# Optimization experiments

Measured on AMD Instinct MI355X. Metric: run time of the kernel, lower is better.

## Reference

```python
import jax, jax.numpy as jnp
import numpy as np
import math

D = 1024
B, S = 8, 2048


def setup_inputs() -> dict:
    key = jax.random.key(0)
    ks = jax.random.split(key, 8)
    q = jax.random.normal(ks[0], (B, S, D), dtype=jnp.float32)
    k = jax.random.normal(ks[1], (B, S, D), dtype=jnp.float32)
    v1 = jax.random.normal(ks[2], (B, S, D), dtype=jnp.float32)
    mask = jax.random.normal(ks[3], (1, S, S), dtype=jnp.float32)
    # Linear params: torch Linear stores W as [out, in]; init ~ U(-1/sqrt(in), 1/sqrt(in))
    lim = 1.0 / math.sqrt(D)
    W1 = jax.random.uniform(ks[4], (D, D), jnp.float32, -lim, lim)
    b1 = jax.random.uniform(ks[5], (D,), jnp.float32, -lim, lim)
    W2 = jax.random.uniform(ks[6], (D, D), jnp.float32, -lim, lim)
    b2 = jax.random.uniform(ks[7], (D,), jnp.float32, -lim, lim)
    return {"q": q, "k": k, "v1": v1, "mask": mask,
            "W1": W1, "b1": b1, "W2": W2, "b2": b2}


def _proj(x, W1, b1, W2, b2):
    # linear2(linear1(x)); torch Linear: x @ W.T + b
    h = jnp.einsum('bsd,od->bso', x, W1) + b1
    return jnp.einsum('bsd,od->bso', h, W2) + b2


def reference(q, k, v1, mask, W1, b1, W2, b2):
    qp = _proj(q, W1, b1, W2, b2)          # [B,S,D]
    kp = _proj(k, W1, b1, W2, b2)          # [B,S,D]
    scale = 1.0 / math.sqrt(qp.shape[-1])
    qk = jnp.einsum('bqd,bkd->bqk', qp, kp) * scale  # [B,S,S]
    qk = qk + mask                          # broadcast [1,S,S]
    attn = jax.nn.softmax(qk, axis=-1)
    return jnp.einsum('bqk,bkd->bqd', attn, v1)  # [B,S,D]
```

## Files before the change

kernel.cpp:

```cpp
#include <hip/hip_runtime.h>
#include <hip/hip_bf16.h>

typedef __hip_bfloat16 bf16;
typedef __bf16 bf16x8 __attribute__((ext_vector_type(8)));
typedef float f32x4 __attribute__((ext_vector_type(4)));

constexpr int Bn = 8, Sn = 2048, Dn = 1024;
constexpr int BM = 256, BN = 256, BK = 64;

__global__ void cast_f32_bf16_k(const float* __restrict__ x, bf16* __restrict__ y, int n) {
  int i = (blockIdx.x * blockDim.x + threadIdx.x) * 4;
  if (i >= n) return;
  float4 f = *reinterpret_cast<const float4*>(x + i);
  bf16 tmp[4] = {__float2bfloat16(f.x), __float2bfloat16(f.y),
                 __float2bfloat16(f.z), __float2bfloat16(f.w)};
  *reinterpret_cast<short4*>(y + i) = *reinterpret_cast<const short4*>(tmp);
}

__global__ void transpose_cast_v_k(const float* __restrict__ v, bf16* __restrict__ vt) {
  __shared__ float tile[32][33];
  const int s0 = blockIdx.x * 32, d0 = blockIdx.y * 32, b = blockIdx.z;
  const float* src = v + (size_t)b * Sn * Dn;
  bf16* dst = vt + (size_t)b * Dn * Sn;
  const int tx = threadIdx.x & 31, ty = threadIdx.x >> 5;
  #pragma unroll
  for (int i = 0; i < 4; ++i) {
    int s = ty + i * 8;
    tile[s][tx] = src[(size_t)(s0 + s) * Dn + d0 + tx];
  }
  __syncthreads();
  #pragma unroll
  for (int i = 0; i < 4; ++i) {
    int d = ty + i * 8;
    dst[(size_t)(d0 + d) * Sn + s0 + tx] = __float2bfloat16(tile[tx][d]);
  }
}

#define SBAR()  asm volatile("s_barrier" ::: "memory")
#define LGKM0() asm volatile("s_waitcnt lgkmcnt(0)" ::: "memory")
#define VM4()   asm volatile("s_waitcnt vmcnt(4)" ::: "memory")
#define VM0()   asm volatile("s_waitcnt vmcnt(0)" ::: "memory")

#define QUAD(ms, ns) do {                                                     \
    __builtin_amdgcn_s_setprio(1);                                            \
    _Pragma("unroll")                                                         \
    for (int kk = 0; kk < 2; ++kk)                                            \
      _Pragma("unroll")                                                       \
      for (int mi4 = 0; mi4 < 4; ++mi4)                                       \
        _Pragma("unroll")                                                     \
        for (int n2 = 0; n2 < 2; ++n2)                                        \
          acc[(ms)*4+mi4][(ns)*2+n2] =                                        \
            __builtin_amdgcn_mfma_f32_16x16x32_bf16(                          \
              aF[mi4][kk], bF[(ns)*2+n2][kk],                                 \
              acc[(ms)*4+mi4][(ns)*2+n2], 0, 0, 0);                           \
    __builtin_amdgcn_s_setprio(0);                                            \
  } while (0)

#define RD_A(buf, ms) do {                                                    \
    _Pragma("unroll")                                                         \
    for (int mi4 = 0; mi4 < 4; ++mi4) {                                       \
      aF[mi4][0] = *reinterpret_cast<const bf16x8*>(                          \
          pA0 + ((buf)*32768 + (ms)*8192 + mi4*2048));                        \
      aF[mi4][1] = *reinterpret_cast<const bf16x8*>(                          \
          pA1 + ((buf)*32768 + (ms)*8192 + mi4*2048));                        \
    }                                                                         \
  } while (0)

#define RD_B(buf, ns) do {                                                    \
    _Pragma("unroll")                                                         \
    for (int j = 0; j < 2; ++j) {                                             \
      bF[(ns)*2+j][0] = *reinterpret_cast<const bf16x8*>(                     \
          pB0 + ((buf)*32768 + (ns)*4096 + j*2048));                          \
      bF[(ns)*2+j][1] = *reinterpret_cast<const bf16x8*>(                     \
          pB1 + ((buf)*32768 + (ns)*4096 + j*2048));                          \
    }                                                                         \
  } while (0)

template<int EPI>
__global__ __launch_bounds__(512, 2)
void gemm256_k(const bf16* __restrict__ A, const bf16* __restrict__ BT,
               void* __restrict__ Cv, const float* __restrict__ aux,
               int N, int K, long long sAz, long long sBz, long long sCz,
               float scale, int gx, int gy)
{
  __shared__ __align__(128) bf16 sh[4 * 16384];

  const int nwg = (int)gridDim.x;
  const int flat = (int)blockIdx.x;
  const int swz = (flat & 7) * (nwg >> 3) + (flat >> 3);
  const int tn = swz % gx;
  const int rem = swz / gx;
  const int tm = rem % gy;
  const int z  = rem / gy;

  const int t = threadIdx.x, w = t >> 6, lane = t & 63;
  const int wm = w >> 2, wn = w & 3;
  const int fr = lane & 15, kg = lane >> 4;
  const int m0 = tm * BM, n0 = tn * BN;
  const bf16* Abase = A + (size_t)z * sAz + (size_t)m0 * K;
  const bf16* Bbase = BT + (size_t)z * sBz + (size_t)n0 * K;

  f32x4 acc[8][4];
  const f32x4 fz = {0.f, 0.f, 0.f, 0.f};
  #pragma unroll
  for (int i = 0; i < 8; ++i)
    #pragma unroll
    for (int j = 0; j < 4; ++j) acc[i][j] = fz;
  bf16x8 aF[4][2], bF[4][2];

  const char* shB = (const char*)sh;
  const int m48 = (fr & 3) << 4;
  const int m64 = (fr & 4) << 4;
  const int aoff0 = (wm * 128 + fr) * 128 + ((kg * 16) ^ m48) + m64;
  const int boff0 = 65536 + (wn * 64 + fr) * 128 + ((kg * 16) ^ m48) + m64;
  const char* pA0 = shB + aoff0;
  const char* pA1 = shB + (aoff0 ^ 64);
  const char* pB0 = shB + boff0;
  const char* pB1 = shB + (boff0 ^ 64);

  int gOff[2];
  #pragma unroll
  for (int i = 0; i < 2; ++i) {
    const int slot = i * 512 + w * 64 + lane;
    const int row = slot >> 3;
    const int cb = (slot & 7) ^ (row & 7);
    gOff[i] = row * K + cb * 8;
  }
  auto stage = [&](int dstElemBase, const bf16* gbase, int half, int kt) {
    const bf16* g0 = gbase + (size_t)(half * 128) * K + (size_t)kt * BK;
    bf16* db = (bf16*)sh + dstElemBase + half * 8192;
    #pragma unroll
    for (int i = 0; i < 2; ++i) {
      __builtin_amdgcn_global_load_lds(
          (__attribute__((address_space(1))) void*)(g0 + gOff[i]),
          (__attribute__((address_space(3))) void*)(db + (i * 512 + w * 64) * 8),
          16, 0, 0);
    }
  };

  const int NT = K / BK;
  stage(32768, Bbase, 0, 0); stage(32768, Bbase, 1, 0);
  stage(0,     Abase, 0, 0); stage(0,     Abase, 1, 0);
  stage(49152, Bbase, 0, 1); stage(49152, Bbase, 1, 1);
  VM4();
  SBAR();

  for (int T = 0; T < NT; T += 2) {
    const bool last = (T + 2 >= NT);
    RD_A(0, 0); RD_B(0, 0);
    stage(16384, Abase, 0, T + 1);
    SBAR(); LGKM0(); QUAD(0, 0); SBAR();
    RD_B(0, 1);
    stage(16384, Abase, 1, T + 1);
    SBAR(); LGKM0(); QUAD(0, 1); SBAR();
    RD_A(0, 1);
    if (!last) stage(32768, Bbase, 0, T + 2);
    SBAR(); LGKM0(); QUAD(1, 0); SBAR();
    if (!last) stage(32768, Bbase, 1, T + 2);
    SBAR(); LGKM0(); QUAD(1, 1);
    if (last) { VM0(); } else { VM4(); }
    SBAR();
    RD_A(1, 0); RD_B(1, 0);
    if (!last) stage(0, Abase, 0, T + 2);
    SBAR(); LGKM0(); QUAD(0, 0); SBAR();
    RD_B(1, 1);
    if (!last) stage(0, Abase, 1, T + 2);
    SBAR(); LGKM0(); QUAD(0, 1); SBAR();
    RD_A(1, 1);
    if (!last) stage(49152, Bbase, 0, T + 3);
    SBAR(); LGKM0(); QUAD(1, 0); SBAR();
    if (!last) stage(49152, Bbase, 1, T + 3);
    SBAR(); LGKM0(); QUAD(1, 1);
    if (!last) { VM4(); }
    SBAR();
  }

  const int or0 = kg * 4;
  if constexpr (EPI == 0) {
    bf16* C = (bf16*)Cv + (size_t)z * sCz;
    #pragma unroll
    for (int mi = 0; mi < 8; ++mi)
      #pragma unroll
      for (int r = 0; r < 4; ++r) {
        const int row = m0 + wm * 128 + mi * 16 + or0 + r;
        #pragma unroll
        for (int ni = 0; ni < 4; ++ni) {
          const int col = n0 + wn * 64 + ni * 16 + fr;
          C[(size_t)row * N + col] = __float2bfloat16(acc[mi][ni][r] + aux[col]);
        }
      }
  } else if constexpr (EPI == 1) {
    bf16* C = (bf16*)Cv + (size_t)z * sCz;
    #pragma unroll
    for (int mi = 0; mi < 8; ++mi)
      #pragma unroll
      for (int r = 0; r < 4; ++r) {
        const int row = m0 + wm * 128 + mi * 16 + or0 + r;
        #pragma unroll
        for (int ni = 0; ni < 4; ++ni) {
          const int col = n0 + wn * 64 + ni * 16 + fr;
          float v = acc[mi][ni][r] * scale + aux[(size_t)row * N + col];
          C[(size_t)row * N + col] = __float2bfloat16(v);
        }
      }
  } else {
    float* C = (float*)Cv + (size_t)z * sCz;
    #pragma unroll
    for (int mi = 0; mi < 8; ++mi)
      #pragma unroll
      for (int r = 0; r < 4; ++r) {
        const int row = m0 + wm * 128 + mi * 16 + or0 + r;
        #pragma unroll
        for (int ni = 0; ni < 4; ++ni) {
          const int col = n0 + wn * 64 + ni * 16 + fr;
          C[(size_t)row * N + col] = acc[mi][ni][r];
        }
      }
  }
}

__global__ __launch_bounds__(256)
void softmax_rows_k(bf16* __restrict__ sc) {
  const size_t row = blockIdx.x;
  bf16* p = sc + row * (size_t)Sn;
  const int t = threadIdx.x;
  unsigned short raw[8];
  *reinterpret_cast<int4*>(raw) = *reinterpret_cast<const int4*>(p + t * 8);
  float x[8];
  float m = -1e30f;
  #pragma unroll
  for (int j = 0; j < 8; ++j) {
    x[j] = __uint_as_float(((unsigned)raw[j]) << 16);
    m = fmaxf(m, x[j]);
  }
  #pragma unroll
  for (int off = 32; off >= 1; off >>= 1) m = fmaxf(m, __shfl_xor(m, off));
  __shared__ float sred[4], ssum[4];
  const int w = t >> 6;
  if ((t & 63) == 0) sred[w] = m;
  __syncthreads();
  m = fmaxf(fmaxf(sred[0], sred[1]), fmaxf(sred[2], sred[3]));
  float e[8], s = 0.f;
  #pragma unroll
  for (int j = 0; j < 8; ++j) { e[j] = __expf(x[j] - m); s += e[j]; }
  #pragma unroll
  for (int off = 32; off >= 1; off >>= 1) s += __shfl_xor(s, off);
  if ((t & 63) == 0) ssum[w] = s;
  __syncthreads();
  s = (ssum[0] + ssum[1]) + (ssum[2] + ssum[3]);
  const float inv = 1.f / s;
  unsigned short o[8];
  #pragma unroll
  for (int j = 0; j < 8; ++j) {
    bf16 hv = __float2bfloat16(e[j] * inv);
    o[j] = *reinterpret_cast<unsigned short*>(&hv);
  }
  *reinterpret_cast<int4*>(p + t * 8) = *reinterpret_cast<const int4*>(o);
}

extern "C" void kernel_launch(void* const* d_in, const int* in_sizes, int n_in,
                              void* d_out, int out_size, void* d_ws, size_t ws_size,
                              hipStream_t stream) {
  const float* q    = (const float*)d_in[0];
  const float* k    = (const float*)d_in[1];
  const float* v1   = (const float*)d_in[2];
  const float* mask = (const float*)d_in[3];
  const float* W1   = (const float*)d_in[4];
  const float* b1   = (const float*)d_in[5];
  const float* W2   = (const float*)d_in[6];
  const float* b2   = (const float*)d_in[7];
  float* out = (float*)d_out;

  const size_t nQKD = (size_t)Bn * Sn * Dn;
  char* ws = (char*)d_ws;
  bf16* qkb = (bf16*)ws;
  bf16* qb  = qkb;
  bf16* kb  = qkb + nQKD;
  bf16* vtb = qkb + 2 * nQKD;
  bf16* hb  = vtb + nQKD;
  bf16* w1b = hb + 2 * nQKD;
  bf16* w2b = w1b + (size_t)Dn * Dn;
  bf16* scb = w2b + (size_t)Dn * Dn;

  dim3 blk(256);
  const int nQK = (int)nQKD;
  cast_f32_bf16_k<<<dim3(nQK / 4 / 256), blk, 0, stream>>>(q, qb, nQK);
  cast_f32_bf16_k<<<dim3(nQK / 4 / 256), blk, 0, stream>>>(k, kb, nQK);
  cast_f32_bf16_k<<<dim3(Dn * Dn / 4 / 256), blk, 0, stream>>>(W1, w1b, Dn * Dn);
  cast_f32_bf16_k<<<dim3(Dn * Dn / 4 / 256), blk, 0, stream>>>(W2, w2b, Dn * Dn);
  transpose_cast_v_k<<<dim3(Sn / 32, Dn / 32, Bn), blk, 0, stream>>>(v1, vtb);

  const int M2 = 2 * Bn * Sn;
  dim3 gblk(512);
  gemm256_k<0><<<dim3(4 * (M2 / BM)), gblk, 0, stream>>>(
      qkb, w1b, hb, b1, Dn, Dn, 0, 0, 0, 1.f, 4, M2 / BM);
  gemm256_k<0><<<dim3(4 * (M2 / BM)), gblk, 0, stream>>>(
      hb, w2b, qkb, b2, Dn, Dn, 0, 0, 0, 1.f, 4, M2 / BM);
  gemm256_k<1><<<dim3(8 * 8 * Bn), gblk, 0, stream>>>(
      qb, kb, scb, mask, Sn, Dn,
      (long long)Sn * Dn, (long long)Sn * Dn, (long long)Sn * Sn, 0.03125f, 8, 8);
  softmax_rows_k<<<dim3(Bn * Sn), blk, 0, stream>>>(scb);
  gemm256_k<2><<<dim3(4 * 8 * Bn), gblk, 0, stream>>>(
      scb, vtb, out, nullptr, Dn, Sn,
      (long long)Sn * Sn, (long long)Dn * Sn, (long long)Sn * Dn, 1.f, 4, 8);
}
```

Baseline: 376.7 us.

## Shrink GEMM tiles to 128x128 with simple double-buffered pipeline

Replaces the 256x256 GEMM tile with a 128x128 tile and swaps the fine-grained quad-split schedule for a simple two-stage double buffer: prefetch the next K tile, compute the current one, then wait on all loads. It halves LDS use and raises occupancy to 4 workgroups per CU, with 4x more workgroups per launch for better CU fill. In exchange, per-tile arithmetic intensity drops, global and L2 traffic rises, and full vmcnt(0) waits each iteration may expose load latency.

```diff
diff --git a/kernel.cpp b/kernel.cpp
--- a/kernel.cpp
+++ b/kernel.cpp
@@ -6,7 +6,7 @@
 typedef float f32x4 __attribute__((ext_vector_type(4)));
 
 constexpr int Bn = 8, Sn = 2048, Dn = 1024;
-constexpr int BM = 256, BN = 256, BK = 64;
+constexpr int BM = 128, BN = 128, BK = 64;
 
 __global__ void cast_f32_bf16_k(const float* __restrict__ x, bf16* __restrict__ y, int n) {
   int i = (blockIdx.x * blockDim.x + threadIdx.x) * 4;
@@ -38,10 +38,9 @@
 
 #define SBAR()  asm volatile("s_barrier" ::: "memory")
 #define LGKM0() asm volatile("s_waitcnt lgkmcnt(0)" ::: "memory")
-#define VM4()   asm volatile("s_waitcnt vmcnt(4)" ::: "memory")
 #define VM0()   asm volatile("s_waitcnt vmcnt(0)" ::: "memory")
 
-#define QUAD(ms, ns) do {                                                     \
+#define MFMA16() do {                                                         \
     __builtin_amdgcn_s_setprio(1);                                            \
     _Pragma("unroll")                                                         \
     for (int kk = 0; kk < 2; ++kk)                                            \
@@ -49,41 +48,41 @@
       for (int mi4 = 0; mi4 < 4; ++mi4)                                       \
         _Pragma("unroll")                                                     \
         for (int n2 = 0; n2 < 2; ++n2)                                        \
-          acc[(ms)*4+mi4][(ns)*2+n2] =                                        \
-            __builtin_amdgcn_mfma_f32_16x16x32_bf16(                          \
-              aF[mi4][kk], bF[(ns)*2+n2][kk],                                 \
-              acc[(ms)*4+mi4][(ns)*2+n2], 0, 0, 0);                           \
+          acc[mi4][n2] = __builtin_amdgcn_mfma_f32_16x16x32_bf16(             \
+              aF[mi4][kk], bF[n2][kk], acc[mi4][n2], 0, 0, 0);                \
     __builtin_amdgcn_s_setprio(0);                                            \
   } while (0)
 
-#define RD_A(buf, ms) do {                                                    \
+#define ITER(cur, T) do {                                                     \
+    const bool pf = (T) + 1 < NT;                                             \
+    if (pf) {                                                                 \
+      stage2((1 - (cur)) * 32768,         Abase, (T) + 1);                    \
+      stage2((1 - (cur)) * 32768 + 16384, Bbase, (T) + 1);                    \
+    }                                                                         \
     _Pragma("unroll")                                                         \
     for (int mi4 = 0; mi4 < 4; ++mi4) {                                       \
-      aF[mi4][0] = *reinterpret_cast<const bf16x8*>(                          \
-          pA0 + ((buf)*32768 + (ms)*8192 + mi4*2048));                        \
-      aF[mi4][1] = *reinterpret_cast<const bf16x8*>(                          \
-          pA1 + ((buf)*32768 + (ms)*8192 + mi4*2048));                        \
+      aF[mi4][0] = *reinterpret_cast<const bf16x8*>(pA0 + (cur)*32768 + mi4*2048); \
+      aF[mi4][1] = *reinterpret_cast<const bf16x8*>(pA1 + (cur)*32768 + mi4*2048); \
     }                                                                         \
-  } while (0)
-
-#define RD_B(buf, ns) do {                                                    \
     _Pragma("unroll")                                                         \
     for (int j = 0; j < 2; ++j) {                                             \
-      bF[(ns)*2+j][0] = *reinterpret_cast<const bf16x8*>(                     \
-          pB0 + ((buf)*32768 + (ns)*4096 + j*2048));                          \
-      bF[(ns)*2+j][1] = *reinterpret_cast<const bf16x8*>(                     \
-          pB1 + ((buf)*32768 + (ns)*4096 + j*2048));                          \
+      bF[j][0] = *reinterpret_cast<const bf16x8*>(pB0 + (cur)*32768 + j*2048); \
+      bF[j][1] = *reinterpret_cast<const bf16x8*>(pB1 + (cur)*32768 + j*2048); \
     }                                                                         \
+    LGKM0();                                                                  \
+    MFMA16();                                                                 \
+    if (pf) VM0();                                                            \
+    SBAR();                                                                   \
   } while (0)
 
 template<int EPI>
-__global__ __launch_bounds__(512, 2)
-void gemm256_k(const bf16* __restrict__ A, const bf16* __restrict__ BT,
+__global__ __launch_bounds__(512, 4)
+void gemm128_k(const bf16* __restrict__ A, const bf16* __restrict__ BT,
                void* __restrict__ Cv, const float* __restrict__ aux,
                int N, int K, long long sAz, long long sBz, long long sCz,
                float scale, int gx, int gy)
 {
-  __shared__ __align__(128) bf16 sh[4 * 16384];
+  __shared__ __align__(128) bf16 sh[2 * 16384];
 
   const int nwg = (int)gridDim.x;
   const int flat = (int)blockIdx.x;
@@ -100,19 +99,17 @@
   const bf16* Abase = A + (size_t)z * sAz + (size_t)m0 * K;
   const bf16* Bbase = BT + (size_t)z * sBz + (size_t)n0 * K;
 
-  f32x4 acc[8][4];
+  f32x4 acc[4][2];
   const f32x4 fz = {0.f, 0.f, 0.f, 0.f};
   #pragma unroll
-  for (int i = 0; i < 8; ++i)
-    #pragma unroll
-    for (int j = 0; j < 4; ++j) acc[i][j] = fz;
-  bf16x8 aF[4][2], bF[4][2];
+  for (int i = 0; i < 4; ++i) { acc[i][0] = fz; acc[i][1] = fz; }
+  bf16x8 aF[4][2], bF[2][2];
 
   const char* shB = (const char*)sh;
-  const int m48 = (fr & 3) << 4;
-  const int m64 = (fr & 4) << 4;
-  const int aoff0 = (wm * 128 + fr) * 128 + ((kg * 16) ^ m48) + m64;
-  const int boff0 = 65536 + (wn * 64 + fr) * 128 + ((kg * 16) ^ m48) + m64;
+  const int swzlo = (fr & 3) << 4;
+  const int swzhi = (fr & 4) << 4;
+  const int aoff0 = (wm * 64 + fr) * 128 + ((kg * 16) ^ swzlo) + swzhi;
+  const int boff0 = 16384 + (wn * 32 + fr) * 128 + ((kg * 16) ^ swzlo) + swzhi;
   const char* pA0 = shB + aoff0;
   const char* pA1 = shB + (aoff0 ^ 64);
   const char* pB0 = shB + boff0;
@@ -126,94 +123,68 @@
     const int cb = (slot & 7) ^ (row & 7);
     gOff[i] = row * K + cb * 8;
   }
-  auto stage = [&](int dstElemBase, const bf16* gbase, int half, int kt) {
-    const bf16* g0 = gbase + (size_t)(half * 128) * K + (size_t)kt * BK;
-    bf16* db = (bf16*)sh + dstElemBase + half * 8192;
+  auto stage2 = [&](int dstByte, const bf16* gbase, int kt) {
+    const bf16* g0 = gbase + (size_t)kt * BK;
+    char* db = (char*)sh + dstByte;
     #pragma unroll
     for (int i = 0; i < 2; ++i) {
       __builtin_amdgcn_global_load_lds(
           (__attribute__((address_space(1))) void*)(g0 + gOff[i]),
-          (__attribute__((address_space(3))) void*)(db + (i * 512 + w * 64) * 8),
+          (__attribute__((address_space(3))) void*)(db + (i * 512 + w * 64) * 16),
           16, 0, 0);
     }
   };
 
   const int NT = K / BK;
-  stage(32768, Bbase, 0, 0); stage(32768, Bbase, 1, 0);
-  stage(0,     Abase, 0, 0); stage(0,     Abase, 1, 0);
-  stage(49152, Bbase, 0, 1); stage(49152, Bbase, 1, 1);
-  VM4();
+  stage2(0,     Abase, 0);
+  stage2(16384, Bbase, 0);
+  VM0();
   SBAR();
 
   for (int T = 0; T < NT; T += 2) {
-    const bool last = (T + 2 >= NT);
-    RD_A(0, 0); RD_B(0, 0);
-    stage(16384, Abase, 0, T + 1);
-    SBAR(); LGKM0(); QUAD(0, 0); SBAR();
-    RD_B(0, 1);
-    stage(16384, Abase, 1, T + 1);
-    SBAR(); LGKM0(); QUAD(0, 1); SBAR();
-    RD_A(0, 1);
-    if (!last) stage(32768, Bbase, 0, T + 2);
-    SBAR(); LGKM0(); QUAD(1, 0); SBAR();
-    if (!last) stage(32768, Bbase, 1, T + 2);
-    SBAR(); LGKM0(); QUAD(1, 1);
-    if (last) { VM0(); } else { VM4(); }
-    SBAR();
-    RD_A(1, 0); RD_B(1, 0);
-    if (!last) stage(0, Abase, 0, T + 2);
-    SBAR(); LGKM0(); QUAD(0, 0); SBAR();
-    RD_B(1, 1);
-    if (!last) stage(0, Abase, 1, T + 2);
-    SBAR(); LGKM0(); QUAD(0, 1); SBAR();
-    RD_A(1, 1);
-    if (!last) stage(49152, Bbase, 0, T + 3);
-    SBAR(); LGKM0(); QUAD(1, 0); SBAR();
-    if (!last) stage(49152, Bbase, 1, T + 3);
-    SBAR(); LGKM0(); QUAD(1, 1);
-    if (!last) { VM4(); }
-    SBAR();
+    ITER(0, T);
+    ITER(1, T + 1);
   }
 
   const int or0 = kg * 4;
   if constexpr (EPI == 0) {
     bf16* C = (bf16*)Cv + (size_t)z * sCz;
     #pragma unroll
-    for (int mi = 0; mi < 8; ++mi)
+    for (int mi = 0; mi < 4; ++mi)
       #pragma unroll
       for (int r = 0; r < 4; ++r) {
-        const int row = m0 + wm * 128 + mi * 16 + or0 + r;
+        const int row = m0 + wm * 64 + mi * 16 + or0 + r;
         #pragma unroll
-        for (int ni = 0; ni < 4; ++ni) {
-          const int col = n0 + wn * 64 + ni * 16 + fr;
-          C[(size_t)row * N + col] = __float2bfloat16(acc[mi][ni][r] + aux[col]);
+        for (int nj = 0; nj < 2; ++nj) {
+          const int col = n0 + wn * 32 + nj * 16 + fr;
+          C[(size_t)row * N + col] = __float2bfloat16(acc[mi][nj][r] + aux[col]);
         }
       }
   } else if constexpr (EPI == 1) {
     bf16* C = (bf16*)Cv + (size_t)z * sCz;
     #pragma unroll
-    for (int mi = 0; mi < 8; ++mi)
+    for (int mi = 0; mi < 4; ++mi)
       #pragma unroll
       for (int r = 0; r < 4; ++r) {
-        const int row = m0 + wm * 128 + mi * 16 + or0 + r;
+        const int row = m0 + wm * 64 + mi * 16 + or0 + r;
         #pragma unroll
-        for (int ni = 0; ni < 4; ++ni) {
-          const int col = n0 + wn * 64 + ni * 16 + fr;
-          float v = acc[mi][ni][r] * scale + aux[(size_t)row * N + col];
+        for (int nj = 0; nj < 2; ++nj) {
+          const int col = n0 + wn * 32 + nj * 16 + fr;
+          float v = acc[mi][nj][r] * scale + aux[(size_t)row * N + col];
           C[(size_t)row * N + col] = __float2bfloat16(v);
         }
       }
   } else {
     float* C = (float*)Cv + (size_t)z * sCz;
     #pragma unroll
-    for (int mi = 0; mi < 8; ++mi)
+    for (int mi = 0; mi < 4; ++mi)
       #pragma unroll
       for (int r = 0; r < 4; ++r) {
-        const int row = m0 + wm * 128 + mi * 16 + or0 + r;
+        const int row = m0 + wm * 64 + mi * 16 + or0 + r;
         #pragma unroll
-        for (int ni = 0; ni < 4; ++ni) {
-          const int col = n0 + wn * 64 + ni * 16 + fr;
-          C[(size_t)row * N + col] = acc[mi][ni][r];
+        for (int nj = 0; nj < 2; ++nj) {
+          const int col = n0 + wn * 32 + nj * 16 + fr;
+          C[(size_t)row * N + col] = acc[mi][nj][r];
         }
       }
   }
@@ -292,15 +263,15 @@
 
   const int M2 = 2 * Bn * Sn;
   dim3 gblk(512);
-  gemm256_k<0><<<dim3(4 * (M2 / BM)), gblk, 0, stream>>>(
-      qkb, w1b, hb, b1, Dn, Dn, 0, 0, 0, 1.f, 4, M2 / BM);
-  gemm256_k<0><<<dim3(4 * (M2 / BM)), gblk, 0, stream>>>(
-      hb, w2b, qkb, b2, Dn, Dn, 0, 0, 0, 1.f, 4, M2 / BM);
-  gemm256_k<1><<<dim3(8 * 8 * Bn), gblk, 0, stream>>>(
+  gemm128_k<0><<<dim3((Dn / BN) * (M2 / BM)), gblk, 0, stream>>>(
+      qkb, w1b, hb, b1, Dn, Dn, 0, 0, 0, 1.f, Dn / BN, M2 / BM);
+  gemm128_k<0><<<dim3((Dn / BN) * (M2 / BM)), gblk, 0, stream>>>(
+      hb, w2b, qkb, b2, Dn, Dn, 0, 0, 0, 1.f, Dn / BN, M2 / BM);
+  gemm128_k<1><<<dim3(16 * 16 * Bn), gblk, 0, stream>>>(
       qb, kb, scb, mask, Sn, Dn,
-      (long long)Sn * Dn, (long long)Sn * Dn, (long long)Sn * Sn, 0.03125f, 8, 8);
+      (long long)Sn * Dn, (long long)Sn * Dn, (long long)Sn * Sn, 0.03125f, 16, 16);
   softmax_rows_k<<<dim3(Bn * Sn), blk, 0, stream>>>(scb);
-  gemm256_k<2><<<dim3(4 * 8 * Bn), gblk, 0, stream>>>(
+  gemm128_k<2><<<dim3(8 * 16 * Bn), gblk, 0, stream>>>(
       scb, vtb, out, nullptr, Dn, Sn,
-      (long long)Sn * Sn, (long long)Dn * Sn, (long long)Sn * Dn, 1.f, 4, 8);
-}
+      (long long)Sn * Sn, (long long)Dn * Sn, (long long)Sn * Dn, 1.f, 8, 16);
+}
```

After: 402.4 us. +6.8%, slower.
